# Kernel tuning notes

Hardware: AMD Instinct MI355X
Metric: run time of the kernel (lower is better)

Reference implementation:

```python
import jax, jax.numpy as jnp
import numpy as np


def setup_inputs() -> dict:
    key = jax.random.key(0)
    k1, k2 = jax.random.split(key)
    B, N, M = 8, 8192, 8192
    input1 = jax.random.normal(k1, (B, N, 3), dtype=jnp.float32)
    input2 = jax.random.normal(k2, (B, M, 3), dtype=jnp.float32)
    return {"input1": input1, "input2": input2}


def _chamfer(xyz1, xyz2):
    # xyz1: [B, N, 3], xyz2: [B, M, 3]
    sq1 = jnp.sum(xyz1 * xyz1, axis=-1)              # [B, N]
    sq2 = jnp.sum(xyz2 * xyz2, axis=-1)              # [B, M]
    cross = jnp.einsum("bnd,bmd->bnm", xyz1, xyz2)  # [B, N, M]
    d = sq1[:, :, None] + sq2[:, None, :] - 2.0 * cross
    dist1 = jnp.min(d, axis=2)  # [B, N] nearest in xyz2 for each pt of xyz1
    dist2 = jnp.min(d, axis=1)  # [B, M]
    return dist1, dist2


def reference(input1, input2):
    return _chamfer(input1, input2)
```

## Files before the change

kernel.cpp:

```cpp
#include <hip/hip_runtime.h>


typedef __attribute__((ext_vector_type(8))) short  s16x8;
typedef __attribute__((ext_vector_type(16))) float f32x16;
typedef unsigned int u32;

#define TSLICE 512
#define QPB    512
#define QPW    128

__device__ inline u32 umin3(u32 a, u32 b, u32 c) {
    const u32 t = a < b ? a : b;
    return t < c ? t : c;
}

__device__ inline f32x16 mfma_chain(const s16x8 a, const s16x8 b,
                                    const f32x16 c, u32& chain) {
    f32x16 d;
    asm("v_mfma_f32_32x32x16_bf16 %0, %2, %3, %4\n\t"
        "s_nop 7\n\ts_nop 7\n\ts_nop 7"
        : "=&v"(d), "+v"(chain) : "v"(a), "v"(b), "v"(c));
    return d;
}

__device__ inline unsigned int bf16bits(float v, float &hival) {
    unsigned int u = __float_as_uint(v);
    unsigned int r = (u + 0x7FFFu + ((u >> 16) & 1u)) >> 16;
    hival = __uint_as_float(r << 16);
    return r;
}

__global__ __launch_bounds__(256)
void pack_all_kernel(const float* __restrict__ in1, const float* __restrict__ in2,
                     ushort* __restrict__ A1, ushort* __restrict__ B1, float* __restrict__ S1,
                     ushort* __restrict__ A2, ushort* __restrict__ B2, float* __restrict__ S2,
                     unsigned int* __restrict__ out, int P1, int P2) {
    const int g = blockIdx.x * 256 + threadIdx.x;
    if (g >= P1 + P2) return;
    out[g] = 0x7F7F7F7Fu;

    const float* src; ushort* pA; ushort* pB; float* sq; int p;
    if (g < P1) { src = in1; pA = A1; pB = B1; sq = S1; p = g; }
    else        { src = in2; pA = A2; pB = B2; sq = S2; p = g - P1; }

    const float x = src[3*p+0], y = src[3*p+1], z = src[3*p+2];
    float xhf, xlf, yhf, ylf, zhf, zlf, shf, tmp;
    const ushort xh = (ushort)bf16bits(x, xhf);
    const ushort xl = (ushort)bf16bits(x - xhf, xlf);
    const ushort yh = (ushort)bf16bits(y, yhf);
    const ushort yl = (ushort)bf16bits(y - yhf, ylf);
    const ushort zh = (ushort)bf16bits(z, zhf);
    const ushort zl = (ushort)bf16bits(z - zhf, zlf);
    const float s = fmaf(x, x, fmaf(y, y, z * z));
    const ushort sh = (ushort)bf16bits(s, shf);
    const ushort sl = (ushort)bf16bits(s - shf, tmp);
    const ushort m2xh = (ushort)bf16bits(-2.0f * xhf, tmp);
    const ushort m2xl = (ushort)bf16bits(-2.0f * xlf, tmp);
    const ushort m2yh = (ushort)bf16bits(-2.0f * yhf, tmp);
    const ushort m2yl = (ushort)bf16bits(-2.0f * ylf, tmp);
    const ushort m2zh = (ushort)bf16bits(-2.0f * zhf, tmp);
    const ushort m2zl = (ushort)bf16bits(-2.0f * zlf, tmp);
    const ushort ONE  = 0x3F80;
    const ushort BIAS = 0x4400;

    const s16x8 a0 = {(short)m2xh,(short)m2xl,(short)m2xh,(short)m2xl,
                      (short)m2yh,(short)m2yl,(short)m2yh,(short)m2yl};
    const s16x8 a1 = {(short)m2zh,(short)m2zl,(short)m2zh,(short)m2zl,
                      (short)sh,  (short)sl,  (short)BIAS, 0};
    const s16x8 b0 = {(short)xh,(short)xh,(short)xl,(short)xl,
                      (short)yh,(short)yh,(short)yl,(short)yl};
    const s16x8 b1 = {(short)zh,(short)zh,(short)zl,(short)zl,
                      (short)ONE,(short)ONE,(short)ONE, 0};

    s16x8* A8 = (s16x8*)pA;
    s16x8* B8 = (s16x8*)pB;
    const int c0 = (p & ~31) * 2 + (p & 31);
    A8[c0]      = a0;
    A8[c0 + 32] = a1;
    B8[2*p]     = b0;
    B8[2*p + 1] = b1;
    sq[p] = s;
}

__global__ __launch_bounds__(256, 4)
void chamfer_mfma_kernel(const ushort* __restrict__ Ad1, const ushort* __restrict__ Bd1,
                         const float*  __restrict__ Sd1, unsigned int* __restrict__ Od1,
                         const ushort* __restrict__ Ad2, const ushort* __restrict__ Bd2,
                         const float*  __restrict__ Sd2, unsigned int* __restrict__ Od2,
                         int Np, int Mp) {
    __shared__ s16x8 lds8[TSLICE * 2];
    const int z = blockIdx.z;
    const ushort* pA  = z ? Ad2 : Ad1;
    const ushort* pB  = z ? Bd2 : Bd1;
    const float*  sqq = z ? Sd2 : Sd1;
    unsigned int* out = z ? Od2 : Od1;

    const int tid  = threadIdx.x;
    const int lane = tid & 63;
    const int wid  = tid >> 6;
    const int qblock = blockIdx.x * QPB;
    const int b = qblock / Np;
    const size_t gchunk = ((size_t)b * Mp + (size_t)blockIdx.y * TSLICE) * 2;
    const s16x8* gA = (const s16x8*)pA + gchunk;
    for (int i = tid; i < TSLICE * 2; i += 256) lds8[i] = gA[i];

    const int qw = qblock + wid * QPW;
    s16x8 bfr[4];
    #pragma unroll
    for (int f = 0; f < 4; ++f) {
        const int q = qw + f * 32 + (lane & 31);
        bfr[f] = *(const s16x8*)(pB + (size_t)q * 16 + (size_t)(lane >> 5) * 8);
    }
    __syncthreads();

    f32x16 cz = {0.f,0.f,0.f,0.f,0.f,0.f,0.f,0.f,
                 0.f,0.f,0.f,0.f,0.f,0.f,0.f,0.f};
    asm("" : "+v"(cz));

    u32 bests[4] = {0x7F7F7F7Fu, 0x7F7F7F7Fu, 0x7F7F7F7Fu, 0x7F7F7F7Fu};

    const int NT = TSLICE / 32;
    s16x8 a = lds8[lane];
    for (int t = 0; t < NT; ++t) {
        const int tn = (t + 1 < NT) ? (t + 1) : t;
        const s16x8 an = lds8[tn * 64 + lane];
        #pragma unroll
        for (int f = 0; f < 4; ++f) {
            const f32x16 d = mfma_chain(a, bfr[f], cz, bests[(f + 3) & 3]);
            const u32 m0 = umin3(__float_as_uint(d[0]),  __float_as_uint(d[1]),  __float_as_uint(d[2]));
            const u32 m1 = umin3(__float_as_uint(d[3]),  __float_as_uint(d[4]),  __float_as_uint(d[5]));
            const u32 m2 = umin3(__float_as_uint(d[6]),  __float_as_uint(d[7]),  __float_as_uint(d[8]));
            const u32 m3 = umin3(__float_as_uint(d[9]),  __float_as_uint(d[10]), __float_as_uint(d[11]));
            const u32 m4 = umin3(__float_as_uint(d[12]), __float_as_uint(d[13]), __float_as_uint(d[14]));
            const u32 m5 = umin3(m0, m1, __float_as_uint(d[15]));
            const u32 m6 = umin3(m2, m3, m4);
            bests[f] = umin3(m5, m6, bests[f]);
        }
        a = an;
    }

    #pragma unroll
    for (int f = 0; f < 4; ++f) {
        u32 bu = bests[f];
        const u32 other = __shfl_xor(bu, 32);
        bu = bu < other ? bu : other;
        const int q = qw + f * 32 + (lane & 31);
        float v = (__uint_as_float(bu) - 512.0f) + sqq[q];
        v = fmaxf(v, 0.0f);
        if (lane < 32) atomicMin(out + q, __float_as_uint(v));
    }
}

#define FSLICE 512
#define FROWS  512
__global__ __launch_bounds__(256)
void chamfer_dir_kernel(const float* __restrict__ P, const float* __restrict__ Q,
                        unsigned int* __restrict__ out, int Np, int Mp) {
    __shared__ float4 lds[FSLICE];
    const int tid = threadIdx.x;
    const int rowBase = blockIdx.x * FROWS;
    const int b = rowBase / Np;
    const int slice0 = blockIdx.y * FSLICE;
    const float* qs = Q + ((size_t)b * Mp + slice0) * 3;
    #pragma unroll
    for (int i = tid; i < FSLICE; i += 256) {
        const float x = qs[3*i+0], y = qs[3*i+1], z = qs[3*i+2];
        lds[i] = make_float4(x, y, z, fmaf(x, x, fmaf(y, y, z * z)));
    }
    const int q0 = rowBase + tid, q1 = q0 + 256;
    const float* p0 = P + (size_t)q0 * 3;
    const float* p1 = P + (size_t)q1 * 3;
    const float x0=p0[0], y0=p0[1], z0=p0[2], x1=p1[0], y1=p1[1], z1=p1[2];
    const float m2x0=-2*x0, m2y0=-2*y0, m2z0=-2*z0, m2x1=-2*x1, m2y1=-2*y1, m2z1=-2*z1;
    const float sqp0 = fmaf(x0,x0,fmaf(y0,y0,z0*z0));
    const float sqp1 = fmaf(x1,x1,fmaf(y1,y1,z1*z1));
    __syncthreads();
    float best0 = 3.0e38f, best1 = 3.0e38f;
    #pragma unroll 4
    for (int j = 0; j < FSLICE; j += 2) {
        const float4 a = lds[j], c = lds[j+1];
        const float d00 = fmaf(m2x0,a.x,fmaf(m2y0,a.y,fmaf(m2z0,a.z,a.w)));
        const float d01 = fmaf(m2x0,c.x,fmaf(m2y0,c.y,fmaf(m2z0,c.z,c.w)));
        best0 = fminf(fminf(d00,d01), best0);
        const float d10 = fmaf(m2x1,a.x,fmaf(m2y1,a.y,fmaf(m2z1,a.z,a.w)));
        const float d11 = fmaf(m2x1,c.x,fmaf(m2y1,c.y,fmaf(m2z1,c.z,c.w)));
        best1 = fminf(fminf(d10,d11), best1);
    }
    atomicMin(out + q0, __float_as_uint(fmaxf(best0 + sqp0, 0.f)));
    atomicMin(out + q1, __float_as_uint(fmaxf(best1 + sqp1, 0.f)));
}

extern "C" void kernel_launch(void* const* d_in, const int* in_sizes, int n_in,
                              void* d_out, int out_size, void* d_ws, size_t ws_size,
                              hipStream_t stream) {
    const float* in1 = (const float*)d_in[0];
    const float* in2 = (const float*)d_in[1];
    const int B = 8;
    const int N = in_sizes[0] / (B * 3);
    const int M = in_sizes[1] / (B * 3);
    const int P1 = B * N, P2 = B * M;
    unsigned int* out = (unsigned int*)d_out;

    const size_t packBytes1 = (size_t)P1 * 32, packBytes2 = (size_t)P2 * 32;
    const size_t need = 2*packBytes1 + 2*packBytes2 + (size_t)(P1+P2)*4;

    if (ws_size >= need && N == M) {
        char* w = (char*)d_ws;
        ushort* A1 = (ushort*)(w);
        ushort* B1 = (ushort*)(w + packBytes1);
        ushort* A2 = (ushort*)(w + 2*packBytes1);
        ushort* B2 = (ushort*)(w + 2*packBytes1 + packBytes2);
        float*  S1 = (float*) (w + 2*packBytes1 + 2*packBytes2);
        float*  S2 = (float*) (w + 2*packBytes1 + 2*packBytes2 + (size_t)P1*4);

        pack_all_kernel<<<(P1 + P2 + 255)/256, 256, 0, stream>>>(
            in1, in2, A1, B1, S1, A2, B2, S2, out, P1, P2);

        dim3 g(P1 / QPB, M / TSLICE, 2);
        chamfer_mfma_kernel<<<g, 256, 0, stream>>>(
            A2, B1, S1, out,
            A1, B2, S2, out + P1,
            N, M);
    } else {
        hipMemsetAsync(d_out, 0x7F, (size_t)out_size * sizeof(float), stream);
        dim3 g1(P1 / FROWS, M / FSLICE);
        chamfer_dir_kernel<<<g1, 256, 0, stream>>>(in1, in2, out, N, M);
        dim3 g2(P2 / FROWS, N / FSLICE);
        chamfer_dir_kernel<<<g2, 256, 0, stream>>>(in2, in1, out + P1, M, N);
    }
}
```

Before: 50.02 us.

## Overlap MFMA execution with min-reduction of previous tile result in inline asm

Replaces the MFMA-then-wait pattern with a software-pipelined inline-asm block. Each MFMA is issued and then the v_min3 reduction of the previous MFMA's output runs while the new one executes, which cuts most of the s_nop padding. A final epilogue reduces the last result into bests[3]. It also drops the occupancy hint from launch_bounds, which gives the compiler more registers for the extra live accumulator but may lower waves per SIMD.

```diff
diff --git a/kernel.cpp b/kernel.cpp
--- a/kernel.cpp
+++ b/kernel.cpp
@@ -14,12 +14,27 @@
     return t < c ? t : c;
 }
 
-__device__ inline f32x16 mfma_chain(const s16x8 a, const s16x8 b,
-                                    const f32x16 c, u32& chain) {
+__device__ inline f32x16 mfma_fold(const s16x8 a, const s16x8 b, const f32x16 c,
+                                   const f32x16 p, u32& best) {
     f32x16 d;
-    asm("v_mfma_f32_32x32x16_bf16 %0, %2, %3, %4\n\t"
-        "s_nop 7\n\ts_nop 7\n\ts_nop 7"
-        : "=&v"(d), "+v"(chain) : "v"(a), "v"(b), "v"(c));
+    u32 t0, t1, t2, t3, t4;
+    asm("v_mfma_f32_32x32x16_bf16 %0, %7, %8, %9\n\t"
+        "v_min3_u32 %2, %10, %11, %12\n\t"
+        "v_min3_u32 %3, %13, %14, %15\n\t"
+        "v_min3_u32 %4, %16, %17, %18\n\t"
+        "v_min3_u32 %5, %19, %20, %21\n\t"
+        "v_min3_u32 %6, %22, %23, %24\n\t"
+        "v_min3_u32 %2, %2, %3, %25\n\t"
+        "v_min3_u32 %4, %4, %5, %6\n\t"
+        "v_min3_u32 %1, %2, %4, %1\n\t"
+        "s_nop 7"
+        : "=&v"(d), "+v"(best),
+          "=&v"(t0), "=&v"(t1), "=&v"(t2), "=&v"(t3), "=&v"(t4)
+        : "v"(a), "v"(b), "v"(c),
+          "v"(p[0]),  "v"(p[1]),  "v"(p[2]),  "v"(p[3]),
+          "v"(p[4]),  "v"(p[5]),  "v"(p[6]),  "v"(p[7]),
+          "v"(p[8]),  "v"(p[9]),  "v"(p[10]), "v"(p[11]),
+          "v"(p[12]), "v"(p[13]), "v"(p[14]), "v"(p[15]));
     return d;
 }
 
@@ -82,7 +97,7 @@
     sq[p] = s;
 }
 
-__global__ __launch_bounds__(256, 4)
+__global__ __launch_bounds__(256)
 void chamfer_mfma_kernel(const ushort* __restrict__ Ad1, const ushort* __restrict__ Bd1,
                          const float*  __restrict__ Sd1, unsigned int* __restrict__ Od1,
                          const ushort* __restrict__ Ad2, const ushort* __restrict__ Bd2,
@@ -119,24 +134,32 @@
 
     u32 bests[4] = {0x7F7F7F7Fu, 0x7F7F7F7Fu, 0x7F7F7F7Fu, 0x7F7F7F7Fu};
 
+    const float SENT = __uint_as_float(0x7F7F7F7Fu);
+    f32x16 dprev = {SENT,SENT,SENT,SENT,SENT,SENT,SENT,SENT,
+                    SENT,SENT,SENT,SENT,SENT,SENT,SENT,SENT};
+
     const int NT = TSLICE / 32;
     s16x8 a = lds8[lane];
     for (int t = 0; t < NT; ++t) {
         const int tn = (t + 1 < NT) ? (t + 1) : t;
         const s16x8 an = lds8[tn * 64 + lane];
-        #pragma unroll
-        for (int f = 0; f < 4; ++f) {
-            const f32x16 d = mfma_chain(a, bfr[f], cz, bests[(f + 3) & 3]);
-            const u32 m0 = umin3(__float_as_uint(d[0]),  __float_as_uint(d[1]),  __float_as_uint(d[2]));
-            const u32 m1 = umin3(__float_as_uint(d[3]),  __float_as_uint(d[4]),  __float_as_uint(d[5]));
-            const u32 m2 = umin3(__float_as_uint(d[6]),  __float_as_uint(d[7]),  __float_as_uint(d[8]));
-            const u32 m3 = umin3(__float_as_uint(d[9]),  __float_as_uint(d[10]), __float_as_uint(d[11]));
-            const u32 m4 = umin3(__float_as_uint(d[12]), __float_as_uint(d[13]), __float_as_uint(d[14]));
-            const u32 m5 = umin3(m0, m1, __float_as_uint(d[15]));
-            const u32 m6 = umin3(m2, m3, m4);
-            bests[f] = umin3(m5, m6, bests[f]);
-        }
+        dprev = mfma_fold(a, bfr[0], cz, dprev, bests[3]);
+        dprev = mfma_fold(a, bfr[1], cz, dprev, bests[0]);
+        dprev = mfma_fold(a, bfr[2], cz, dprev, bests[1]);
+        dprev = mfma_fold(a, bfr[3], cz, dprev, bests[2]);
         a = an;
+    }
+
+    asm("s_nop 7\n\ts_nop 7\n\ts_nop 7" : "+v"(dprev));
+    {
+        const u32 m0 = umin3(__float_as_uint(dprev[0]),  __float_as_uint(dprev[1]),  __float_as_uint(dprev[2]));
+        const u32 m1 = umin3(__float_as_uint(dprev[3]),  __float_as_uint(dprev[4]),  __float_as_uint(dprev[5]));
+        const u32 m2 = umin3(__float_as_uint(dprev[6]),  __float_as_uint(dprev[7]),  __float_as_uint(dprev[8]));
+        const u32 m3 = umin3(__float_as_uint(dprev[9]),  __float_as_uint(dprev[10]), __float_as_uint(dprev[11]));
+        const u32 m4 = umin3(__float_as_uint(dprev[12]), __float_as_uint(dprev[13]), __float_as_uint(dprev[14]));
+        const u32 m5 = umin3(m0, m1, __float_as_uint(dprev[15]));
+        const u32 m6 = umin3(m2, m3, m4);
+        bests[3] = umin3(m5, m6, bests[3]);
     }
 
     #pragma unroll
```

Result: no change. 49.15 us (-1.7%).
